# Kernel tuning notes

Measured on AMD Instinct MI355X. Metric: run time of the kernel, lower is better.

The kernel has to match this reference:

```python
import jax, jax.numpy as jnp
import numpy as np

NUM_HEADS = 8
EPS = 1e-12  # tf.nn.l2_normalize epsilon


def _l2_normalize(t):
    # tf.nn.l2_normalize: x * rsqrt(max(sum(x^2), eps)) along last axis
    sq = jnp.sum(t * t, axis=-1, keepdims=True)
    return t * jax.lax.rsqrt(jnp.maximum(sq, EPS))


def setup_inputs() -> dict:
    key = jax.random.key(0)
    ks = jax.random.split(key, 4)
    B, N, C = 8, 4096, 512
    x = jax.random.normal(ks[0], (B, N, C), dtype=jnp.float32)
    w_qkv = jax.random.normal(ks[1], (C, 3 * C), dtype=jnp.float32) * (C ** -0.5)
    b_qkv = jnp.zeros((3 * C,), dtype=jnp.float32)
    w_proj = jax.random.normal(ks[2], (C, C), dtype=jnp.float32) * (C ** -0.5)
    b_proj = jnp.zeros((C,), dtype=jnp.float32)
    return {"x": x, "w_qkv": w_qkv, "b_qkv": b_qkv, "w_proj": w_proj, "b_proj": b_proj}


def reference(x, w_qkv, b_qkv, w_proj, b_proj):
    B, N, C = x.shape
    h = NUM_HEADS
    d = C // h
    scale = d ** -0.5
    qkv = x @ w_qkv + b_qkv                        # [B,N,3C]
    qkv = qkv.reshape(B, N, 3, h, d)
    qkv = jnp.transpose(qkv, (2, 0, 3, 1, 4))      # [3,B,h,N,d]
    q, k, v = qkv[0], qkv[1], qkv[2]
    q = _l2_normalize(q) * scale
    k = _l2_normalize(k)
    # channel-wise attention: q^T k over tokens -> [B,h,d,d]
    attn = jnp.einsum('bhnd,bhne->bhde', q, k)
    attn = jax.nn.softmax(attn, axis=-1)
    out = jnp.einsum('bhnd,bhde->bhne', v, attn)   # [B,h,N,d]
    out = jnp.transpose(out, (0, 2, 1, 3)).reshape(B, N, C)
    out = out @ w_proj + b_proj
    return out
```

## Files before the change

kernel.cpp:

```cpp
#include <hip/hip_runtime.h>
#include <stdint.h>

#define NB 8
#define NN 4096
#define NC 512
#define NH 8

typedef __bf16 bf16x8 __attribute__((ext_vector_type(8)));
typedef float floatx4 __attribute__((ext_vector_type(4)));

__device__ __forceinline__ unsigned short f2bf(float f) {
  union { float f; unsigned u; } v; v.f = f;
  return (unsigned short)((v.u + 0x7fffu + ((v.u >> 16) & 1u)) >> 16);
}
__device__ __forceinline__ float bf2f(unsigned short s) {
  union { unsigned u; float f; } v; v.u = ((unsigned)s) << 16;
  return v.f;
}
__device__ __forceinline__ float2 bfp2f(unsigned u) {
  union { unsigned x; float f; } lo, hi;
  lo.x = u << 16; hi.x = u & 0xffff0000u;
  return make_float2(lo.f, hi.f);
}

__device__ __forceinline__ void async_ld16(void* lds, const void* g) {
  auto* gp = (const __attribute__((address_space(1))) unsigned int*)(uintptr_t)g;
  auto* lp = (__attribute__((address_space(3))) unsigned int*)(uintptr_t)lds;
  __builtin_amdgcn_global_load_lds(gp, lp, 16, 0, 0);
}

__global__ __launch_bounds__(256) void k_convert(const float* __restrict__ src,
                                                 unsigned short* __restrict__ dst, int n) {
  int i = (blockIdx.x * 256 + threadIdx.x) * 4;
  if (i >= n) return;
  float4 v = *(const float4*)(src + i);
  ushort4 o;
  o.x = f2bf(v.x); o.y = f2bf(v.y); o.z = f2bf(v.z); o.w = f2bf(v.w);
  *(ushort4*)(dst + i) = o;
}

__global__ __launch_bounds__(256) void k_transpose_cvt(const float* __restrict__ w,
                                                       unsigned short* __restrict__ wt) {
  int id = blockIdx.x * 256 + threadIdx.x;
  int nn = id >> 9, kk = id & 511;
  wt[id] = f2bf(w[kk * 1536 + nn]);
}

__global__ __launch_bounds__(256) void k_gemm_qkv(const unsigned short* __restrict__ A,
                                                  const unsigned short* __restrict__ Bt,
                                                  const float* __restrict__ bias,
                                                  unsigned short* __restrict__ Cq) {
  const int K = 512, LDA = 512, LDB = 512, LDC = 1536;
  int m0 = blockIdx.x * 128, n0 = blockIdx.y * 128;
  int tid = threadIdx.x;
  int lane = tid & 63, w = tid >> 6;
  int wm = (w & 1) * 64, wn = (w >> 1) * 64;
  int quad = lane >> 4, rr = lane & 15;
  int r8 = lane >> 3;
  int cg = lane & 7;
  int cgs = cg ^ r8;
  const int swz = rr & 7;

  __shared__ __align__(16) unsigned short Als[128][64];
  __shared__ __align__(16) unsigned short Bls[128][64];

  floatx4 acc[4][4];
#pragma unroll
  for (int i = 0; i < 4; i++)
#pragma unroll
    for (int j = 0; j < 4; j++) acc[i][j] = (floatx4){0.f, 0.f, 0.f, 0.f};

  for (int k0 = 0; k0 < K; k0 += 64) {
#pragma unroll
    for (int i = 0; i < 4; i++) {
      int row = i * 32 + w * 8 + r8;
      async_ld16(&Als[i * 32 + w * 8][0], A + (size_t)(m0 + row) * LDA + k0 + cgs * 8);
      async_ld16(&Bls[i * 32 + w * 8][0], Bt + (size_t)(n0 + row) * LDB + k0 + cgs * 8);
    }
    __syncthreads();
#pragma unroll
    for (int kk = 0; kk < 64; kk += 32) {
      int gb = kk >> 3;
      bf16x8 af[4], bfr[4];
#pragma unroll
      for (int mi = 0; mi < 4; mi++)
        af[mi] = *(const bf16x8*)&Als[wm + mi * 16 + rr][(((gb + quad) ^ swz)) * 8];
#pragma unroll
      for (int ni = 0; ni < 4; ni++)
        bfr[ni] = *(const bf16x8*)&Bls[wn + ni * 16 + rr][(((gb + quad) ^ swz)) * 8];
#pragma unroll
      for (int mi = 0; mi < 4; mi++)
#pragma unroll
        for (int ni = 0; ni < 4; ni++)
          acc[mi][ni] = __builtin_amdgcn_mfma_f32_16x16x32_bf16(af[mi], bfr[ni], acc[mi][ni], 0, 0, 0);
    }
    __syncthreads();
  }
#pragma unroll
  for (int ni = 0; ni < 4; ni++) {
    int col = n0 + wn + ni * 16 + rr;
    float bv = bias[col];
#pragma unroll
    for (int mi = 0; mi < 4; mi++) {
      int rbase = m0 + wm + mi * 16 + quad * 4;
#pragma unroll
      for (int r = 0; r < 4; r++)
        Cq[(size_t)(rbase + r) * LDC + col] = f2bf(acc[mi][ni][r] + bv);
    }
  }
}

__global__ __launch_bounds__(256) void k_attn(const unsigned short* __restrict__ QKV,
                                              float* __restrict__ logits_p) {
  int chunk = blockIdx.x, hh = blockIdx.y, b = blockIdx.z;
  int tid = threadIdx.x, w = tid >> 6, l = tid & 63;
  int quad = l >> 4, rr = l & 15;

  __shared__ __align__(16) unsigned char smem[65536];
  unsigned short* qT = (unsigned short*)smem + w * 2560;
  unsigned short* kT = (unsigned short*)(smem + 20480) + w * 2560;
  float* ps = (float*)smem;

  floatx4 acc[4][4];
#pragma unroll
  for (int i = 0; i < 4; i++)
#pragma unroll
    for (int j = 0; j < 4; j++) acc[i][j] = (floatx4){0.f, 0.f, 0.f, 0.f};

  int t32 = l >> 1;
  int db = (l & 1) * 32;

  for (int s = 0; s < 4; s++) {
    int n = chunk * 512 + w * 128 + s * 32 + t32;
    const unsigned short* basep = QKV + (size_t)(b * 4096 + n) * 1536 + hh * 64 + db;

    float qf[32]; float sq = 0.f;
#pragma unroll
    for (int c = 0; c < 4; c++) {
      uint4 v = *(const uint4*)(basep + c * 8);
      unsigned uu[4] = {v.x, v.y, v.z, v.w};
#pragma unroll
      for (int e = 0; e < 4; e++) {
        float2 f = bfp2f(uu[e]);
        qf[c * 8 + e * 2] = f.x; qf[c * 8 + e * 2 + 1] = f.y;
        sq += f.x * f.x + f.y * f.y;
      }
    }
    sq += __shfl_xor(sq, 1);
    float scq = 0.125f * rsqrtf(fmaxf(sq, 1e-12f));
#pragma unroll
    for (int j = 0; j < 32; j++) qT[(db + j) * 40 + t32] = f2bf(qf[j] * scq);

    float sk = 0.f;
#pragma unroll
    for (int c = 0; c < 4; c++) {
      uint4 v = *(const uint4*)(basep + 512 + c * 8);
      unsigned uu[4] = {v.x, v.y, v.z, v.w};
#pragma unroll
      for (int e = 0; e < 4; e++) {
        float2 f = bfp2f(uu[e]);
        qf[c * 8 + e * 2] = f.x; qf[c * 8 + e * 2 + 1] = f.y;
        sk += f.x * f.x + f.y * f.y;
      }
    }
    sk += __shfl_xor(sk, 1);
    float sck = rsqrtf(fmaxf(sk, 1e-12f));
#pragma unroll
    for (int j = 0; j < 32; j++) kT[(db + j) * 40 + t32] = f2bf(qf[j] * sck);

    bf16x8 af[4], bfr[4];
#pragma unroll
    for (int mi = 0; mi < 4; mi++) af[mi] = *(const bf16x8*)(qT + (mi * 16 + rr) * 40 + quad * 8);
#pragma unroll
    for (int ni = 0; ni < 4; ni++) bfr[ni] = *(const bf16x8*)(kT + (ni * 16 + rr) * 40 + quad * 8);
#pragma unroll
    for (int mi = 0; mi < 4; mi++)
#pragma unroll
      for (int ni = 0; ni < 4; ni++)
        acc[mi][ni] = __builtin_amdgcn_mfma_f32_16x16x32_bf16(af[mi], bfr[ni], acc[mi][ni], 0, 0, 0);
  }

  __syncthreads();
#pragma unroll
  for (int mi = 0; mi < 4; mi++)
#pragma unroll
    for (int ni = 0; ni < 4; ni++)
#pragma unroll
      for (int r = 0; r < 4; r++) {
        int d = mi * 16 + quad * 4 + r, e = ni * 16 + rr;
        ps[w * 4096 + d * 64 + e] = acc[mi][ni][r];
      }
  __syncthreads();
  float* outp = logits_p + ((size_t)(b * 8 + hh) * 8 + chunk) * 4096;
  for (int i = tid; i < 4096; i += 256)
    outp[i] = ps[i] + ps[4096 + i] + ps[8192 + i] + ps[12288 + i];
}

__global__ __launch_bounds__(256) void k_reduce(const float* __restrict__ logits_p,
                                                float* __restrict__ logits) {
  int id = blockIdx.x * 256 + threadIdx.x;
  int bh = id >> 12, r = id & 4095;
  const float* p = logits_p + (size_t)bh * 8 * 4096 + r;
  float s = 0.f;
#pragma unroll
  for (int c = 0; c < 8; c++) s += p[c * 4096];
  logits[id] = s;
}

__global__ __launch_bounds__(256) void k_softmax_m(const float* __restrict__ logits,
                                                   const float* __restrict__ wproj,
                                                   unsigned short* __restrict__ Mt) {
  int cc = blockIdx.x;
  int hh = blockIdx.y, b = blockIdx.z;
  int t = threadIdx.x;
  __shared__ float ls[64][64];
  __shared__ float red[64][4];
  __shared__ float inv[64];
  const float* L = logits + (size_t)(b * 8 + hh) * 4096;
#pragma unroll
  for (int i = 0; i < 16; i++) {
    int id = t + i * 256;
    ls[id >> 6][id & 63] = L[id];
  }
  __syncthreads();
  int row = t >> 2, part = t & 3;
  float mx = -1e30f;
#pragma unroll
  for (int j = 0; j < 16; j++) mx = fmaxf(mx, ls[row][part * 16 + j]);
  red[row][part] = mx;
  __syncthreads();
  if (part == 0) inv[row] = fmaxf(fmaxf(red[row][0], red[row][1]), fmaxf(red[row][2], red[row][3]));
  __syncthreads();
  float rm = inv[row];
  float s = 0.f;
#pragma unroll
  for (int j = 0; j < 16; j++) {
    float e = __expf(ls[row][part * 16 + j] - rm);
    ls[row][part * 16 + j] = e;
    s += e;
  }
  red[row][part] = s;
  __syncthreads();
  if (part == 0) inv[row] = 1.0f / (red[row][0] + red[row][1] + red[row][2] + red[row][3]);
  __syncthreads();
  int cout = cc * 128 + (t & 127);
  for (int rep = 0; rep < 32; rep++) {
    int dd = (t >> 7) + rep * 2;
    float a = 0.f;
#pragma unroll 8
    for (int ee = 0; ee < 64; ee++) a += ls[dd][ee] * wproj[(hh * 64 + ee) * 512 + cout];
    a *= inv[dd];
    Mt[((size_t)b * 512 + cout) * 512 + hh * 64 + dd] = f2bf(a);
  }
}

__global__ __launch_bounds__(256) void k_gemm_out(const unsigned short* __restrict__ QKV,
                                                  const unsigned short* __restrict__ MtAll,
                                                  const float* __restrict__ bias,
                                                  float* __restrict__ Out) {
  const int K = 512, LDA = 1536, LDB = 512, LDC = 512;
  int b = blockIdx.x >> 5;
  int m0 = (blockIdx.x & 31) * 128;
  int n0 = blockIdx.y * 128;
  const unsigned short* A = QKV + (size_t)b * NN * 1536 + 1024;
  const unsigned short* Bt = MtAll + (size_t)b * 512 * 512;
  int tid = threadIdx.x;
  int lane = tid & 63, w = tid >> 6;
  int wm = (w & 1) * 64, wn = (w >> 1) * 64;
  int quad = lane >> 4, rr = lane & 15;
  int r8 = lane >> 3, cg = lane & 7;
  int cgs = cg ^ r8;
  const int swz = rr & 7;

  __shared__ __align__(16) unsigned short Als[128][64];
  __shared__ __align__(16) unsigned short Bls[128][64];

  floatx4 acc[4][4];
#pragma unroll
  for (int i = 0; i < 4; i++)
#pragma unroll
    for (int j = 0; j < 4; j++) acc[i][j] = (floatx4){0.f, 0.f, 0.f, 0.f};

  for (int k0 = 0; k0 < K; k0 += 64) {
#pragma unroll
    for (int i = 0; i < 4; i++) {
      int row = i * 32 + w * 8 + r8;
      async_ld16(&Als[i * 32 + w * 8][0], A + (size_t)(m0 + row) * LDA + k0 + cgs * 8);
      async_ld16(&Bls[i * 32 + w * 8][0], Bt + (size_t)(n0 + row) * LDB + k0 + cgs * 8);
    }
    __syncthreads();
#pragma unroll
    for (int kk = 0; kk < 64; kk += 32) {
      int gb = kk >> 3;
      bf16x8 af[4], bfr[4];
#pragma unroll
      for (int mi = 0; mi < 4; mi++)
        af[mi] = *(const bf16x8*)&Als[wm + mi * 16 + rr][(((gb + quad) ^ swz)) * 8];
#pragma unroll
      for (int ni = 0; ni < 4; ni++)
        bfr[ni] = *(const bf16x8*)&Bls[wn + ni * 16 + rr][(((gb + quad) ^ swz)) * 8];
#pragma unroll
      for (int mi = 0; mi < 4; mi++)
#pragma unroll
        for (int ni = 0; ni < 4; ni++)
          acc[mi][ni] = __builtin_amdgcn_mfma_f32_16x16x32_bf16(af[mi], bfr[ni], acc[mi][ni], 0, 0, 0);
    }
    __syncthreads();
  }
#pragma unroll
  for (int ni = 0; ni < 4; ni++) {
    int col = n0 + wn + ni * 16 + rr;
    float bv = bias[col];
#pragma unroll
    for (int mi = 0; mi < 4; mi++) {
      int rbase = m0 + wm + mi * 16 + quad * 4;
#pragma unroll
      for (int r = 0; r < 4; r++)
        Out[(size_t)b * NN * LDC + (size_t)(rbase + r) * LDC + col] = acc[mi][ni][r] + bv;
    }
  }
}

extern "C" void kernel_launch(void* const* d_in, const int* in_sizes, int n_in,
                              void* d_out, int out_size, void* d_ws, size_t ws_size,
                              hipStream_t stream) {
  const float* x      = (const float*)d_in[0];
  const float* w_qkv  = (const float*)d_in[1];
  const float* b_qkv  = (const float*)d_in[2];
  const float* w_proj = (const float*)d_in[3];
  const float* b_proj = (const float*)d_in[4];
  float* out = (float*)d_out;

  char* ws = (char*)d_ws;
  size_t off = 0;
  auto alloc = [&](size_t bytes) -> void* {
    void* p = ws + off;
    off += (bytes + 255) & ~(size_t)255;
    return p;
  };
  unsigned short* xb       = (unsigned short*)alloc((size_t)NB * NN * NC * 2);
  unsigned short* wT       = (unsigned short*)alloc((size_t)1536 * 512 * 2);
  unsigned short* qkvb     = (unsigned short*)alloc((size_t)NB * NN * 3 * NC * 2);
  float*          logits_p = (float*)alloc((size_t)NB * NH * 8 * 4096 * 4);
  float*          logits   = (float*)alloc((size_t)NB * NH * 4096 * 4);
  unsigned short* Mt       = (unsigned short*)alloc((size_t)NB * 512 * 512 * 2);

  k_convert<<<16384, 256, 0, stream>>>(x, xb, NB * NN * NC);
  k_transpose_cvt<<<3072, 256, 0, stream>>>(w_qkv, wT);
  k_gemm_qkv<<<dim3(256, 12), 256, 0, stream>>>(xb, wT, b_qkv, qkvb);
  k_attn<<<dim3(8, 8, 8), 256, 0, stream>>>(qkvb, logits_p);
  k_reduce<<<1024, 256, 0, stream>>>(logits_p, logits);
  k_softmax_m<<<dim3(4, 8, 8), 256, 0, stream>>>(logits, w_proj, Mt);
  k_gemm_out<<<dim3(256, 4), 256, 0, stream>>>(qkvb, Mt, b_proj, out);
}
```

Before: 320.3 us.

## Tile weight transpose, fuse partial-logit reduction into softmax, restructure attention loads

The weight transpose now goes through a shared-memory tile, so both the global reads and the global writes are coalesced. The attention kernel now loads q and k together, with 8 lanes per token, and reduces the norms with shuffles. It writes into a swizzled LDS layout meant to cut bank conflicts. The separate reduce kernel is removed and its partial-logit sum is folded into the softmax kernel. That kernel now holds w_proj in registers and writes Mt in vector stores. This trades one launch and one global round-trip for more register pressure in the softmax kernel.

Result: faster. 276.5 us (-13.7%).

```diff
diff --git a/kernel.cpp b/kernel.cpp
--- a/kernel.cpp
+++ b/kernel.cpp
@@ -41,9 +41,22 @@
 
 __global__ __launch_bounds__(256) void k_transpose_cvt(const float* __restrict__ w,
                                                        unsigned short* __restrict__ wt) {
-  int id = blockIdx.x * 256 + threadIdx.x;
-  int nn = id >> 9, kk = id & 511;
-  wt[id] = f2bf(w[kk * 1536 + nn]);
+  __shared__ float tile[64][65];
+  int nn0 = blockIdx.x * 64, kk0 = blockIdx.y * 64;
+  int t = threadIdx.x;
+#pragma unroll
+  for (int i = 0; i < 16; i++) {
+    int id = t + i * 256;
+    int r = id >> 6, c = id & 63;
+    tile[c][r] = w[(size_t)(kk0 + r) * 1536 + nn0 + c];
+  }
+  __syncthreads();
+#pragma unroll
+  for (int i = 0; i < 16; i++) {
+    int id = t + i * 256;
+    int rn = id >> 6, ck = id & 63;
+    wt[(size_t)(nn0 + rn) * 512 + kk0 + ck] = f2bf(tile[rn][ck]);
+  }
 }
 
 __global__ __launch_bounds__(256) void k_gemm_qkv(const unsigned short* __restrict__ A,
@@ -56,8 +69,7 @@
   int lane = tid & 63, w = tid >> 6;
   int wm = (w & 1) * 64, wn = (w >> 1) * 64;
   int quad = lane >> 4, rr = lane & 15;
-  int r8 = lane >> 3;
-  int cg = lane & 7;
+  int r8 = lane >> 3, cg = lane & 7;
   int cgs = cg ^ r8;
   const int swz = rr & 7;
 
@@ -117,8 +129,8 @@
   int quad = l >> 4, rr = l & 15;
 
   __shared__ __align__(16) unsigned char smem[65536];
-  unsigned short* qT = (unsigned short*)smem + w * 2560;
-  unsigned short* kT = (unsigned short*)(smem + 20480) + w * 2560;
+  unsigned short* qT = (unsigned short*)smem + w * 5120;
+  unsigned short* kT = qT + 2560;
   float* ps = (float*)smem;
 
   floatx4 acc[4][4];
@@ -127,52 +139,46 @@
 #pragma unroll
     for (int j = 0; j < 4; j++) acc[i][j] = (floatx4){0.f, 0.f, 0.f, 0.f};
 
-  int t32 = l >> 1;
-  int db = (l & 1) * 32;
+  int tok8 = l >> 3;
+  int seg = l & 7;
+  int sw = seg & 3;
 
   for (int s = 0; s < 4; s++) {
-    int n = chunk * 512 + w * 128 + s * 32 + t32;
-    const unsigned short* basep = QKV + (size_t)(b * 4096 + n) * 1536 + hh * 64 + db;
-
-    float qf[32]; float sq = 0.f;
+    int nbase = chunk * 512 + w * 128 + s * 32;
 #pragma unroll
     for (int c = 0; c < 4; c++) {
-      uint4 v = *(const uint4*)(basep + c * 8);
-      unsigned uu[4] = {v.x, v.y, v.z, v.w};
+      int n = nbase + c * 8 + tok8;
+      const unsigned short* p = QKV + (size_t)(b * 4096 + n) * 1536 + hh * 64 + seg * 8;
+      uint4 vq = *(const uint4*)p;
+      uint4 vk = *(const uint4*)(p + 512);
+      unsigned uq[4] = {vq.x, vq.y, vq.z, vq.w};
+      unsigned uk[4] = {vk.x, vk.y, vk.z, vk.w};
+      float qf[8], kf[8], sq = 0.f, sk = 0.f;
 #pragma unroll
       for (int e = 0; e < 4; e++) {
-        float2 f = bfp2f(uu[e]);
-        qf[c * 8 + e * 2] = f.x; qf[c * 8 + e * 2 + 1] = f.y;
-        sq += f.x * f.x + f.y * f.y;
+        float2 f = bfp2f(uq[e]); qf[2 * e] = f.x; qf[2 * e + 1] = f.y; sq += f.x * f.x + f.y * f.y;
+        float2 g = bfp2f(uk[e]); kf[2 * e] = g.x; kf[2 * e + 1] = g.y; sk += g.x * g.x + g.y * g.y;
       }
-    }
-    sq += __shfl_xor(sq, 1);
-    float scq = 0.125f * rsqrtf(fmaxf(sq, 1e-12f));
-#pragma unroll
-    for (int j = 0; j < 32; j++) qT[(db + j) * 40 + t32] = f2bf(qf[j] * scq);
-
-    float sk = 0.f;
-#pragma unroll
-    for (int c = 0; c < 4; c++) {
-      uint4 v = *(const uint4*)(basep + 512 + c * 8);
-      unsigned uu[4] = {v.x, v.y, v.z, v.w};
-#pragma unroll
-      for (int e = 0; e < 4; e++) {
-        float2 f = bfp2f(uu[e]);
-        qf[c * 8 + e * 2] = f.x; qf[c * 8 + e * 2 + 1] = f.y;
-        sk += f.x * f.x + f.y * f.y;
+      sq += __shfl_xor(sq, 1); sq += __shfl_xor(sq, 2); sq += __shfl_xor(sq, 4);
+      sk += __shfl_xor(sk, 1); sk += __shfl_xor(sk, 2); sk += __shfl_xor(sk, 4);
+      float scq = 0.125f * rsqrtf(fmaxf(sq, 1e-12f));
+      float sck = rsqrtf(fmaxf(sk, 1e-12f));
+      int col = ((c ^ sw) << 3) + tok8;
+#pragma unroll
+      for (int j = 0; j < 8; j++) {
+        int dim = seg * 8 + j;
+        qT[dim * 40 + col] = f2bf(qf[j] * scq);
+        kT[dim * 40 + col] = f2bf(kf[j] * sck);
       }
     }
-    sk += __shfl_xor(sk, 1);
-    float sck = rsqrtf(fmaxf(sk, 1e-12f));
-#pragma unroll
-    for (int j = 0; j < 32; j++) kT[(db + j) * 40 + t32] = f2bf(qf[j] * sck);
-
     bf16x8 af[4], bfr[4];
 #pragma unroll
-    for (int mi = 0; mi < 4; mi++) af[mi] = *(const bf16x8*)(qT + (mi * 16 + rr) * 40 + quad * 8);
-#pragma unroll
-    for (int ni = 0; ni < 4; ni++) bfr[ni] = *(const bf16x8*)(kT + (ni * 16 + rr) * 40 + quad * 8);
+    for (int mi = 0; mi < 4; mi++) {
+      int s3 = (mi * 2 + (rr >> 3)) & 3;
+      int off = (mi * 16 + rr) * 40 + ((quad ^ s3) << 3);
+      af[mi] = *(const bf16x8*)(qT + off);
+      bfr[mi] = *(const bf16x8*)(kT + off);
+    }
 #pragma unroll
     for (int mi = 0; mi < 4; mi++)
 #pragma unroll
@@ -196,31 +202,22 @@
     outp[i] = ps[i] + ps[4096 + i] + ps[8192 + i] + ps[12288 + i];
 }
 
-__global__ __launch_bounds__(256) void k_reduce(const float* __restrict__ logits_p,
-                                                float* __restrict__ logits) {
-  int id = blockIdx.x * 256 + threadIdx.x;
-  int bh = id >> 12, r = id & 4095;
-  const float* p = logits_p + (size_t)bh * 8 * 4096 + r;
-  float s = 0.f;
-#pragma unroll
-  for (int c = 0; c < 8; c++) s += p[c * 4096];
-  logits[id] = s;
-}
-
-__global__ __launch_bounds__(256) void k_softmax_m(const float* __restrict__ logits,
+__global__ __launch_bounds__(256) void k_softmax_m(const float* __restrict__ logits_p,
                                                    const float* __restrict__ wproj,
                                                    unsigned short* __restrict__ Mt) {
-  int cc = blockIdx.x;
-  int hh = blockIdx.y, b = blockIdx.z;
+  int cc = blockIdx.x, hh = blockIdx.y, b = blockIdx.z;
   int t = threadIdx.x;
   __shared__ float ls[64][64];
   __shared__ float red[64][4];
   __shared__ float inv[64];
-  const float* L = logits + (size_t)(b * 8 + hh) * 4096;
+  const float* lp = logits_p + (size_t)((b * 8 + hh) * 8) * 4096;
 #pragma unroll
   for (int i = 0; i < 16; i++) {
     int id = t + i * 256;
-    ls[id >> 6][id & 63] = L[id];
+    float s = 0.f;
+#pragma unroll
+    for (int c = 0; c < 8; c++) s += lp[c * 4096 + id];
+    ls[id >> 6][id & 63] = s;
   }
   __syncthreads();
   int row = t >> 2, part = t & 3;
@@ -243,15 +240,27 @@
   __syncthreads();
   if (part == 0) inv[row] = 1.0f / (red[row][0] + red[row][1] + red[row][2] + red[row][3]);
   __syncthreads();
+
   int cout = cc * 128 + (t & 127);
-  for (int rep = 0; rep < 32; rep++) {
-    int dd = (t >> 7) + rep * 2;
+  int half = t >> 7;
+  float wreg[64];
+#pragma unroll
+  for (int ee = 0; ee < 64; ee++) wreg[ee] = wproj[(size_t)(hh * 64 + ee) * 512 + cout];
+  unsigned short ob[32];
+#pragma unroll
+  for (int d2 = 0; d2 < 32; d2++) {
+    int dd = half * 32 + d2;
     float a = 0.f;
-#pragma unroll 8
-    for (int ee = 0; ee < 64; ee++) a += ls[dd][ee] * wproj[(hh * 64 + ee) * 512 + cout];
-    a *= inv[dd];
-    Mt[((size_t)b * 512 + cout) * 512 + hh * 64 + dd] = f2bf(a);
-  }
+#pragma unroll
+    for (int e4 = 0; e4 < 16; e4++) {
+      float4 p4 = *(const float4*)&ls[dd][e4 * 4];
+      a += p4.x * wreg[e4 * 4] + p4.y * wreg[e4 * 4 + 1] + p4.z * wreg[e4 * 4 + 2] + p4.w * wreg[e4 * 4 + 3];
+    }
+    ob[d2] = f2bf(a * inv[dd]);
+  }
+  uint4* dst = (uint4*)(Mt + ((size_t)(b * 512 + cout)) * 512 + hh * 64 + half * 32);
+#pragma unroll
+  for (int i = 0; i < 4; i++) dst[i] = ((const uint4*)ob)[i];
 }
 
 __global__ __launch_bounds__(256) void k_gemm_out(const unsigned short* __restrict__ QKV,
@@ -342,14 +351,12 @@
   unsigned short* wT       = (unsigned short*)alloc((size_t)1536 * 512 * 2);
   unsigned short* qkvb     = (unsigned short*)alloc((size_t)NB * NN * 3 * NC * 2);
   float*          logits_p = (float*)alloc((size_t)NB * NH * 8 * 4096 * 4);
-  float*          logits   = (float*)alloc((size_t)NB * NH * 4096 * 4);
   unsigned short* Mt       = (unsigned short*)alloc((size_t)NB * 512 * 512 * 2);
 
   k_convert<<<16384, 256, 0, stream>>>(x, xb, NB * NN * NC);
-  k_transpose_cvt<<<3072, 256, 0, stream>>>(w_qkv, wT);
+  k_transpose_cvt<<<dim3(24, 8), 256, 0, stream>>>(w_qkv, wT);
   k_gemm_qkv<<<dim3(256, 12), 256, 0, stream>>>(xb, wT, b_qkv, qkvb);
   k_attn<<<dim3(8, 8, 8), 256, 0, stream>>>(qkvb, logits_p);
-  k_reduce<<<1024, 256, 0, stream>>>(logits_p, logits);
-  k_softmax_m<<<dim3(4, 8, 8), 256, 0, stream>>>(logits, w_proj, Mt);
+  k_softmax_m<<<dim3(4, 8, 8), 256, 0, stream>>>(logits_p, w_proj, Mt);
   k_gemm_out<<<dim3(256, 4), 256, 0, stream>>>(qkvb, Mt, b_proj, out);
 }
```
